# Performance work log

Hardware: AMD Instinct MI355X
Metric: run time of the kernel (lower is better)

Reference implementation:

```python
import jax, jax.numpy as jnp
import numpy as np

B, T, I, H = 512, 512, 64, 256


def _gru_layer(x, w_ih, w_hh, b_ih, b_hh):
    # x: [B, T, in]; w_ih: [3H, in]; w_hh: [3H, H]; gate order r, z, n (PyTorch)
    xg = jnp.einsum('bti,gi->btg', x, w_ih) + b_ih  # [B, T, 3H], input projections for all steps
    xg = jnp.swapaxes(xg, 0, 1)  # [T, B, 3H] for scan over time
    h0 = jnp.zeros((x.shape[0], w_hh.shape[1]), dtype=x.dtype)

    def step(h, xg_t):
        hg = h @ w_hh.T + b_hh  # [B, 3H]
        xr, xz, xn = jnp.split(xg_t, 3, axis=-1)
        hr, hz, hn = jnp.split(hg, 3, axis=-1)
        r = jax.nn.sigmoid(xr + hr)
        z = jax.nn.sigmoid(xz + hz)
        n = jnp.tanh(xn + r * hn)
        h_new = (1.0 - z) * n + z * h
        return h_new, h_new

    h_last, ys = jax.lax.scan(step, h0, xg)
    return jnp.swapaxes(ys, 0, 1), h_last  # [B, T, H], [B, H]


def setup_inputs() -> dict:
    key = jax.random.key(0)
    ks = jax.random.split(key, 11)
    s_in = 1.0 / np.sqrt(H)
    x = jax.random.normal(ks[0], (B, T, I), dtype=jnp.float32)
    w_ih0 = jax.random.uniform(ks[1], (3 * H, I), jnp.float32, -s_in, s_in)
    w_hh0 = jax.random.uniform(ks[2], (3 * H, H), jnp.float32, -s_in, s_in)
    b_ih0 = jax.random.uniform(ks[3], (3 * H,), jnp.float32, -s_in, s_in)
    b_hh0 = jax.random.uniform(ks[4], (3 * H,), jnp.float32, -s_in, s_in)
    w_ih1 = jax.random.uniform(ks[5], (3 * H, H), jnp.float32, -s_in, s_in)
    w_hh1 = jax.random.uniform(ks[6], (3 * H, H), jnp.float32, -s_in, s_in)
    b_ih1 = jax.random.uniform(ks[7], (3 * H,), jnp.float32, -s_in, s_in)
    b_hh1 = jax.random.uniform(ks[8], (3 * H,), jnp.float32, -s_in, s_in)
    w_lin = jax.random.uniform(ks[9], (1, H), jnp.float32, -s_in, s_in)
    b_lin = jax.random.uniform(ks[10], (1,), jnp.float32, -s_in, s_in)
    return dict(x=x, w_ih0=w_ih0, w_hh0=w_hh0, b_ih0=b_ih0, b_hh0=b_hh0,
                w_ih1=w_ih1, w_hh1=w_hh1, b_ih1=b_ih1, b_hh1=b_hh1,
                w_lin=w_lin, b_lin=b_lin)


def reference(x, w_ih0, w_hh0, b_ih0, b_hh0, w_ih1, w_hh1, b_ih1, b_hh1, w_lin, b_lin):
    y0, h_last0 = _gru_layer(x, w_ih0, w_hh0, b_ih0, b_hh0)
    # dropout(0.2) between layers is inactive at inference -> identity
    y1, h_last1 = _gru_layer(y0, w_ih1, w_hh1, b_ih1, b_hh1)
    # original uses hn[0] = final hidden of LAYER 0
    logits = (h_last0 @ w_lin.T + b_lin).reshape(-1)  # [B]
    p = jax.nn.sigmoid(logits)
    out = jnp.stack((p, 1.0 - p), axis=1).reshape(-1)  # [2B]
    return out
```

## Files before the change

### kernel.cpp

```cpp
#include <hip/hip_runtime.h>


typedef __attribute__((ext_vector_type(8))) short short8;
typedef __attribute__((ext_vector_type(4))) float floatx4;

#define T_LEN 512
#define I_DIM 64
#define H_DIM 256
#define NB 16
#define NWG 32
#define L2E 1.4426950408889634f

#define HSTATE_OFF 131072
#define XG_OFF     1048576
#define XG_PER_T   786432ull
#define XG_TSTRIDE 393216

__device__ __forceinline__ unsigned short f2bf(float f) {
    union { float f; unsigned u; } v; v.f = f;
    return (unsigned short)((v.u + 0x7FFFu + ((v.u >> 16) & 1u)) >> 16);
}

__device__ __forceinline__ float bf2f(unsigned short u) {
    union { unsigned u; float f; } v; v.u = ((unsigned)u) << 16;
    return v.f;
}

__device__ __forceinline__ short8 pack8v(floatx4 a, floatx4 b) {
    short8 r;
    r[0] = (short)f2bf(a[0]); r[1] = (short)f2bf(a[1]);
    r[2] = (short)f2bf(a[2]); r[3] = (short)f2bf(a[3]);
    r[4] = (short)f2bf(b[0]); r[5] = (short)f2bf(b[1]);
    r[6] = (short)f2bf(b[2]); r[7] = (short)f2bf(b[3]);
    return r;
}

__device__ __forceinline__ short8 pack8s(const float* p, float s) {
    floatx4 a = *(const floatx4*)p;
    floatx4 b = *(const floatx4*)(p + 4);
    short8 r;
    r[0] = (short)f2bf(a[0] * s); r[1] = (short)f2bf(a[1] * s);
    r[2] = (short)f2bf(a[2] * s); r[3] = (short)f2bf(a[3] * s);
    r[4] = (short)f2bf(b[0] * s); r[5] = (short)f2bf(b[1] * s);
    r[6] = (short)f2bf(b[2] * s); r[7] = (short)f2bf(b[3] * s);
    return r;
}

__device__ __forceinline__ float sigm(float a) {
    return 1.0f / (1.0f + __expf(-a));
}

__global__ void cvt_wih_kernel(const float* __restrict__ w,
                               unsigned short* __restrict__ o) {
    int i = blockIdx.x * 256 + threadIdx.x;
    if (i < 6144) {
        const int l  = i & 63;
        const int kx = (i >> 6) & 1;
        const int g  = (i >> 7) % 6;
        const int wv = (i >> 7) / 6;
        const int row = (g >> 1) * 256 + wv * 32 + (g & 1) * 16 + (l & 15);
        const int col = kx * 32 + (l >> 4) * 8;
        const float* p = w + row * I_DIM + col;
        *(short8*)&o[i * 8] = pack8v(*(const floatx4*)p,
                                     *(const floatx4*)(p + 4));
    }
}

__global__ __launch_bounds__(256) void xg_kernel(
    const float* __restrict__ x,
    const unsigned short* __restrict__ wih_bf,
    unsigned short* __restrict__ xg,
    const float* __restrict__ b_ih,
    const float* __restrict__ b_hh,
    int t0)
{
    const int tid  = threadIdx.x;
    const int wv   = tid >> 6;
    const int lane = tid & 63;
    const int m16  = lane & 15;
    const int quad = lane >> 4;
    const int wgb  = blockIdx.x & 31;
    const int tl0  = (blockIdx.x >> 5) * 16 + wv * 4;

    short8 af0[4], af1[4];
    #pragma unroll
    for (int j = 0; j < 4; ++j) {
        const float* xp = x + ((long)(wgb * 16 + m16) * T_LEN + (t0 + tl0 + j))
                              * I_DIM + quad * 8;
        af0[j] = pack8v(*(const floatx4*)xp,        *(const floatx4*)(xp + 4));
        af1[j] = pack8v(*(const floatx4*)(xp + 32), *(const floatx4*)(xp + 36));
    }

    #pragma unroll 1
    for (int wp = 0; wp < 8; ++wp) {
        #pragma unroll 1
        for (int gate = 0; gate < 3; ++gate) {
            const int u0 = wp * 32 + m16;
            float bs0, bs1, sc;
            if (gate < 2) {
                bs0 = b_ih[gate * 256 + u0]      + b_hh[gate * 256 + u0];
                bs1 = b_ih[gate * 256 + u0 + 16] + b_hh[gate * 256 + u0 + 16];
                sc  = L2E;
            } else {
                bs0 = b_ih[512 + u0];
                bs1 = b_ih[512 + u0 + 16];
                sc  = 2.0f * L2E;
            }
            const int gb = (wp * 6 + gate * 2) * 2;
            short8 b00 = *(const short8*)&wih_bf[((gb + 0) * 64 + lane) * 8];
            short8 b01 = *(const short8*)&wih_bf[((gb + 1) * 64 + lane) * 8];
            short8 b10 = *(const short8*)&wih_bf[((gb + 2) * 64 + lane) * 8];
            short8 b11 = *(const short8*)&wih_bf[((gb + 3) * 64 + lane) * 8];
            #pragma unroll
            for (int j = 0; j < 4; ++j) {
                floatx4 a0 = {0, 0, 0, 0}, a1 = {0, 0, 0, 0};
                a0 = __builtin_amdgcn_mfma_f32_16x16x32_bf16(af0[j], b00, a0, 0, 0, 0);
                a0 = __builtin_amdgcn_mfma_f32_16x16x32_bf16(af1[j], b01, a0, 0, 0, 0);
                a1 = __builtin_amdgcn_mfma_f32_16x16x32_bf16(af0[j], b10, a1, 0, 0, 0);
                a1 = __builtin_amdgcn_mfma_f32_16x16x32_bf16(af1[j], b11, a1, 0, 0, 0);
                short8 pk;
                pk[0] = (short)f2bf((a0[0] + bs0) * sc);
                pk[1] = (short)f2bf((a0[1] + bs0) * sc);
                pk[2] = (short)f2bf((a0[2] + bs0) * sc);
                pk[3] = (short)f2bf((a0[3] + bs0) * sc);
                pk[4] = (short)f2bf((a1[0] + bs1) * sc);
                pk[5] = (short)f2bf((a1[1] + bs1) * sc);
                pk[6] = (short)f2bf((a1[2] + bs1) * sc);
                pk[7] = (short)f2bf((a1[3] + bs1) * sc);
                long off = ((((long)(tl0 + j) * 32 + wgb) * 3 + gate) * 512
                            + wp * 64 + lane) * 8;
                *(short8*)&xg[off] = pk;
            }
        }
    }
}

__global__ __launch_bounds__(512, 2) void gru_scan8(
    const unsigned short* __restrict__ xg,
    const float* __restrict__ w_hh,
    const float* __restrict__ b_hh,
    const float* __restrict__ w_lin,
    const float* __restrict__ b_lin,
    float* __restrict__ h_state,
    float* __restrict__ out,
    int t0, int tlen, int last)
{
    __shared__ __align__(16) unsigned short hbf[1024 * 8];

    const int tid  = threadIdx.x;
    const int wave = tid >> 6;
    const int lane = tid & 63;
    const int m16  = lane & 15;
    const int quad = lane >> 4;
    const int wg   = blockIdx.x;

    for (int b = tid; b < 1024; b += 512)
        *(short8*)&hbf[b * 8] = (short8)0;

    float h_old[8] = {0, 0, 0, 0, 0, 0, 0, 0};
    if (t0 > 0) {
        unsigned short* hbn = &hbf[(t0 & 1) * 512 * 8];
        #pragma unroll
        for (int i = 0; i < 2; ++i) {
            #pragma unroll
            for (int r = 0; r < 4; ++r) {
                float v = h_state[(long)(wg * NB + quad * 4 + r) * H_DIM
                                  + wave * 32 + i * 16 + m16];
                h_old[i * 4 + r] = v;
                hbn[(wave * 64 + (i * 2 + (m16 >> 3)) * 16 + quad * 4 + r) * 8
                    + (m16 & 7)] = f2bf(v);
            }
        }
    }

    short8 whh[3][2][8];
    #pragma unroll
    for (int g = 0; g < 3; ++g) {
        const float sc = (g < 2) ? L2E : 2.0f * L2E;
        #pragma unroll
        for (int i = 0; i < 2; ++i) {
            const float* rp = w_hh
                + (long)(g * 256 + wave * 32 + i * 16 + m16) * H_DIM;
            #pragma unroll
            for (int k = 0; k < 8; ++k)
                whh[g][i][k] = pack8s(rp + k * 32 + quad * 8, sc);
        }
    }
    float anb[2];
    anb[0] = 2.0f * L2E * b_hh[512 + wave * 32 + m16];
    anb[1] = 2.0f * L2E * b_hh[512 + wave * 32 + 16 + m16];

    const unsigned short* xgb = xg + (long)wg * 12288 + tid * 8;
    short8 pf0 = *(const short8*)&xgb[0];
    short8 pf1 = *(const short8*)&xgb[4096];
    short8 xnc = *(const short8*)&xgb[8192];
    const unsigned short* xgn = xgb + XG_TSTRIDE;

    if (wave >= 4) __builtin_amdgcn_s_setprio(1);

    __syncthreads();

    #pragma unroll 1
    for (int tt = 0; tt < tlen; ++tt) {
        const int t = t0 + tt;
        floatx4 aR[2], aZ[2], aN[2];
        #pragma unroll
        for (int i = 0; i < 2; ++i) {
            #pragma unroll
            for (int r = 0; r < 4; ++r) {
                aR[i][r] = bf2f((unsigned short)pf0[i * 4 + r]);
                aZ[i][r] = bf2f((unsigned short)pf1[i * 4 + r]);
            }
            aN[i] = (floatx4){anb[i], anb[i], anb[i], anb[i]};
        }
        pf0 = *(const short8*)&xgn[0];
        pf1 = *(const short8*)&xgn[4096];

        const unsigned short* hb = &hbf[(t & 1) * 512 * 8];

        #pragma unroll
        for (int k = 0; k < 8; ++k) {
            short8 af = *(const short8*)&hb[(k * 64 + lane) * 8];
            aR[0] = __builtin_amdgcn_mfma_f32_16x16x32_bf16(af, whh[0][0][k], aR[0], 0, 0, 0);
            aR[1] = __builtin_amdgcn_mfma_f32_16x16x32_bf16(af, whh[0][1][k], aR[1], 0, 0, 0);
            aZ[0] = __builtin_amdgcn_mfma_f32_16x16x32_bf16(af, whh[1][0][k], aZ[0], 0, 0, 0);
            aZ[1] = __builtin_amdgcn_mfma_f32_16x16x32_bf16(af, whh[1][1][k], aZ[1], 0, 0, 0);
        }

        #pragma unroll
        for (int k = 0; k < 8; ++k) {
            short8 af = *(const short8*)&hb[(k * 64 + lane) * 8];
            aN[0] = __builtin_amdgcn_mfma_f32_16x16x32_bf16(af, whh[2][0][k], aN[0], 0, 0, 0);
            aN[1] = __builtin_amdgcn_mfma_f32_16x16x32_bf16(af, whh[2][1][k], aN[1], 0, 0, 0);
        }

        float rr[8], zh[8], omz[8], xf[8];
        #pragma unroll
        for (int i = 0; i < 2; ++i) {
            #pragma unroll
            for (int r = 0; r < 4; ++r) {
                const int e = i * 4 + r;
                rr[e]  = __builtin_amdgcn_rcpf(1.0f + __builtin_amdgcn_exp2f(-aR[i][r]));
                float zz = __builtin_amdgcn_rcpf(1.0f + __builtin_amdgcn_exp2f(-aZ[i][r]));
                zh[e]  = zz * h_old[e];
                omz[e] = 1.0f - zz;
                xf[e]  = bf2f((unsigned short)xnc[i * 4 + r]);
            }
        }

        unsigned short* hbn = &hbf[((t + 1) & 1) * 512 * 8];
        #pragma unroll
        for (int i = 0; i < 2; ++i) {
            float hv0, hv1, hv2, hv3;
            #pragma unroll
            for (int r = 0; r < 4; ++r) {
                const int e = i * 4 + r;
                float av = xf[e] + rr[e] * aN[i][r];
                float tn = 1.0f - 2.0f * __builtin_amdgcn_rcpf(1.0f + __builtin_amdgcn_exp2f(av));
                float hv = omz[e] * tn + zh[e];
                h_old[e] = hv;
                if (r == 0) hv0 = hv; else if (r == 1) hv1 = hv;
                else if (r == 2) hv2 = hv; else hv3 = hv;
            }
            unsigned pk0, pk1;
            asm("v_cvt_pk_bf16_f32 %0, %1, %2" : "=v"(pk0) : "v"(hv0), "v"(hv1));
            asm("v_cvt_pk_bf16_f32 %0, %1, %2" : "=v"(pk1) : "v"(hv2), "v"(hv3));
            unsigned short* wb = &hbn[(wave * 64 + (i * 2 + (m16 >> 3)) * 16
                                       + quad * 4) * 8 + (m16 & 7)];
            wb[0]  = (unsigned short)(pk0 & 0xffffu);
            wb[8]  = (unsigned short)(pk0 >> 16);
            wb[16] = (unsigned short)(pk1 & 0xffffu);
            wb[24] = (unsigned short)(pk1 >> 16);
        }

        xnc = *(const short8*)&xgn[8192];
        if (tt < tlen - 2) xgn += XG_TSTRIDE;

        asm volatile("s_waitcnt lgkmcnt(0)" ::: "memory");
        __builtin_amdgcn_s_barrier();
    }

    if (wave >= 4) __builtin_amdgcn_s_setprio(0);

    #pragma unroll
    for (int i = 0; i < 2; ++i)
        #pragma unroll
        for (int r = 0; r < 4; ++r)
            h_state[(long)(wg * NB + quad * 4 + r) * H_DIM
                    + wave * 32 + i * 16 + m16] = h_old[i * 4 + r];

    if (!last) return;

    __syncthreads();
    float* hfin = (float*)hbf;
    #pragma unroll
    for (int i = 0; i < 2; ++i)
        #pragma unroll
        for (int r = 0; r < 4; ++r)
            hfin[(quad * 4 + r) * 256 + wave * 32 + i * 16 + m16] =
                h_old[i * 4 + r];
    __syncthreads();

    const int m = tid >> 5, j = tid & 31;
    float s = 0.0f;
    #pragma unroll
    for (int c = 0; c < 8; ++c)
        s += hfin[m * 256 + j + c * 32] * w_lin[j + c * 32];
    #pragma unroll
    for (int d = 16; d > 0; d >>= 1) s += __shfl_down(s, d, 32);
    if (j == 0) {
        float p = sigm(s + b_lin[0]);
        const int b = wg * NB + m;
        out[2 * b]     = p;
        out[2 * b + 1] = 1.0f - p;
    }
}

__global__ __launch_bounds__(512, 1) void gru_kernel(
    const float* __restrict__ x,
    const float* __restrict__ w_hh,
    const float* __restrict__ b_ih,
    const float* __restrict__ b_hh,
    const unsigned short* __restrict__ wih_ws,
    const float* __restrict__ w_lin,
    const float* __restrict__ b_lin,
    float* __restrict__ out)
{
    __shared__ __align__(16) unsigned short whn_lds[8192 * 8];
    __shared__ __align__(16) unsigned short hbf[1024 * 8];
    __shared__ __align__(16) unsigned short bias_lds[512 * 8];

    const int tid  = threadIdx.x;
    const int wave = tid >> 6;
    const int lane = tid & 63;
    const int m16  = lane & 15;
    const int quad = lane >> 4;
    const int wg   = blockIdx.x;

    for (int b = tid; b < 8192; b += 512) {
        const int l = b & 63;
        const int k = (b >> 6) & 7;
        const int g = (b >> 9) & 1;
        const int w = b >> 10;
        const int row = 512 + w * 32 + g * 16 + (l & 15);
        const int col = k * 32 + (l >> 4) * 8;
        const float* p = w_hh + row * H_DIM + col;
        *(short8*)&whn_lds[b * 8] = pack8v(*(const floatx4*)p,
                                           *(const floatx4*)(p + 4));
    }
    for (int b = tid; b < 1024; b += 512)
        *(short8*)&hbf[b * 8] = (short8)0;

    {
        const int u0 = wave * 32 + m16, u1 = u0 + 16;
        unsigned short* bl = &bias_lds[tid * 8];
        bl[0] = f2bf(b_ih[u0] + b_hh[u0]);
        bl[1] = f2bf(b_ih[u1] + b_hh[u1]);
        bl[2] = f2bf(b_ih[256 + u0] + b_hh[256 + u0]);
        bl[3] = f2bf(b_ih[256 + u1] + b_hh[256 + u1]);
        bl[4] = f2bf(b_hh[512 + u0]);
        bl[5] = f2bf(b_hh[512 + u1]);
        bl[6] = f2bf(b_ih[512 + u0]);
        bl[7] = f2bf(b_ih[512 + u1]);
    }

    short8 whh[4][8];
    #pragma unroll
    for (int g = 0; g < 4; ++g) {
        const int row = (g >> 1) * 256 + wave * 32 + (g & 1) * 16 + m16;
        const float* rp = w_hh + row * H_DIM;
        #pragma unroll
        for (int k = 0; k < 8; ++k) {
            const float* p = rp + k * 32 + quad * 8;
            whh[g][k] = pack8v(*(const floatx4*)p, *(const floatx4*)(p + 4));
        }
    }

    short8 wi[12];
    {
        const unsigned short* wib = &wih_ws[(wave * 6 * 2 * 64 + lane) * 8];
        #pragma unroll
        for (int j = 0; j < 12; ++j)
            wi[j] = *(const short8*)&wib[j * 64 * 8];
    }

    float h_old[8] = {0, 0, 0, 0, 0, 0, 0, 0};
    const float* xbase = x + (long)(wg * NB + m16) * T_LEN * I_DIM + quad * 8;

    __syncthreads();

    #pragma unroll 1
    for (int t = 0; t < T_LEN; ++t) {
        const float* xt = xbase + t * I_DIM;
        floatx4 x0 = *(const floatx4*)(xt);
        floatx4 x1 = *(const floatx4*)(xt + 4);
        floatx4 x2 = *(const floatx4*)(xt + 32);
        floatx4 x3 = *(const floatx4*)(xt + 36);

        floatx4 acc[4], an[2], xnl[2];
        #pragma unroll
        for (int g = 0; g < 4; ++g) acc[g] = (floatx4){0, 0, 0, 0};
        an[0] = an[1] = xnl[0] = xnl[1] = (floatx4){0, 0, 0, 0};

        const unsigned short* hb  = &hbf[(t & 1) * 512 * 8];
        const unsigned short* wnb = &whn_lds[(wave * 2 * 8 * 64 + lane) * 8];
        #pragma unroll
        for (int k = 0; k < 8; ++k) {
            short8 af  = *(const short8*)&hb[(k * 64 + lane) * 8];
            short8 wn0 = *(const short8*)&wnb[(k * 64) * 8];
            short8 wn1 = *(const short8*)&wnb[((8 + k) * 64) * 8];
            acc[0] = __builtin_amdgcn_mfma_f32_16x16x32_bf16(af, whh[0][k], acc[0], 0, 0, 0);
            acc[1] = __builtin_amdgcn_mfma_f32_16x16x32_bf16(af, whh[1][k], acc[1], 0, 0, 0);
            acc[2] = __builtin_amdgcn_mfma_f32_16x16x32_bf16(af, whh[2][k], acc[2], 0, 0, 0);
            acc[3] = __builtin_amdgcn_mfma_f32_16x16x32_bf16(af, whh[3][k], acc[3], 0, 0, 0);
            an[0]  = __builtin_amdgcn_mfma_f32_16x16x32_bf16(af, wn0, an[0], 0, 0, 0);
            an[1]  = __builtin_amdgcn_mfma_f32_16x16x32_bf16(af, wn1, an[1], 0, 0, 0);
        }

        short8 xa = pack8v(x0, x1);
        acc[0] = __builtin_amdgcn_mfma_f32_16x16x32_bf16(xa, wi[0],  acc[0], 0, 0, 0);
        acc[1] = __builtin_amdgcn_mfma_f32_16x16x32_bf16(xa, wi[2],  acc[1], 0, 0, 0);
        acc[2] = __builtin_amdgcn_mfma_f32_16x16x32_bf16(xa, wi[4],  acc[2], 0, 0, 0);
        acc[3] = __builtin_amdgcn_mfma_f32_16x16x32_bf16(xa, wi[6],  acc[3], 0, 0, 0);
        xnl[0] = __builtin_amdgcn_mfma_f32_16x16x32_bf16(xa, wi[8],  xnl[0], 0, 0, 0);
        xnl[1] = __builtin_amdgcn_mfma_f32_16x16x32_bf16(xa, wi[10], xnl[1], 0, 0, 0);
        xa = pack8v(x2, x3);
        acc[0] = __builtin_amdgcn_mfma_f32_16x16x32_bf16(xa, wi[1],  acc[0], 0, 0, 0);
        acc[1] = __builtin_amdgcn_mfma_f32_16x16x32_bf16(xa, wi[3],  acc[1], 0, 0, 0);
        acc[2] = __builtin_amdgcn_mfma_f32_16x16x32_bf16(xa, wi[5],  acc[2], 0, 0, 0);
        acc[3] = __builtin_amdgcn_mfma_f32_16x16x32_bf16(xa, wi[7],  acc[3], 0, 0, 0);
        xnl[0] = __builtin_amdgcn_mfma_f32_16x16x32_bf16(xa, wi[9],  xnl[0], 0, 0, 0);
        xnl[1] = __builtin_amdgcn_mfma_f32_16x16x32_bf16(xa, wi[11], xnl[1], 0, 0, 0);

        short8 bv = *(const short8*)&bias_lds[tid * 8];
        unsigned short* hbn = &hbf[((t + 1) & 1) * 512 * 8];
        #pragma unroll
        for (int i = 0; i < 2; ++i) {
            #pragma unroll
            for (int r = 0; r < 4; ++r) {
                const int idx = i * 4 + r;
                float rr = sigm(acc[i][r]     + bf2f((unsigned short)bv[i]));
                float zz = sigm(acc[2 + i][r] + bf2f((unsigned short)bv[2 + i]));
                float av = xnl[i][r] + bf2f((unsigned short)bv[6 + i])
                         + rr * (an[i][r] + bf2f((unsigned short)bv[4 + i]));
                float nn = 1.0f - 2.0f / (1.0f + __expf(2.0f * av));
                float hn = (1.0f - zz) * nn + zz * h_old[idx];
                h_old[idx] = hn;
                hbn[(wave * 64 + (i * 2 + (m16 >> 3)) * 16 + quad * 4 + r) * 8
                    + (m16 & 7)] = f2bf(hn);
            }
        }
        __syncthreads();
    }

    __syncthreads();
    float* hfin = (float*)hbf;
    #pragma unroll
    for (int i = 0; i < 2; ++i)
        #pragma unroll
        for (int r = 0; r < 4; ++r)
            hfin[(quad * 4 + r) * 256 + wave * 32 + i * 16 + m16] =
                h_old[i * 4 + r];
    __syncthreads();

    const int m = tid >> 5, j = tid & 31;
    float s = 0.0f;
    #pragma unroll
    for (int c = 0; c < 8; ++c)
        s += hfin[m * 256 + j + c * 32] * w_lin[j + c * 32];
    #pragma unroll
    for (int d = 16; d > 0; d >>= 1) s += __shfl_down(s, d, 32);
    if (j == 0) {
        float p = sigm(s + b_lin[0]);
        const int b = wg * NB + m;
        out[2 * b]     = p;
        out[2 * b + 1] = 1.0f - p;
    }
}

extern "C" void kernel_launch(void* const* d_in, const int* in_sizes, int n_in,
                              void* d_out, int out_size, void* d_ws, size_t ws_size,
                              hipStream_t stream) {
    const float* x     = (const float*)d_in[0];
    const float* w_ih0 = (const float*)d_in[1];
    const float* w_hh0 = (const float*)d_in[2];
    const float* b_ih0 = (const float*)d_in[3];
    const float* b_hh0 = (const float*)d_in[4];
    const float* w_lin = (const float*)d_in[9];
    const float* b_lin = (const float*)d_in[10];
    float* out = (float*)d_out;

    unsigned short* wih_bf = (unsigned short*)d_ws;
    cvt_wih_kernel<<<24, 256, 0, stream>>>(w_ih0, wih_bf);

    int Tc = 0;
    for (int c = 512; c >= 32; c >>= 1)
        if (ws_size >= XG_OFF + (size_t)c * XG_PER_T) { Tc = c; break; }

    if (Tc) {
        float* h_state = (float*)((char*)d_ws + HSTATE_OFF);
        unsigned short* xg = (unsigned short*)((char*)d_ws + XG_OFF);
        for (int t0 = 0; t0 < T_LEN; t0 += Tc) {
            xg_kernel<<<32 * (Tc / 16), 256, 0, stream>>>(x, wih_bf, xg,
                                                          b_ih0, b_hh0, t0);
            gru_scan8<<<NWG, 512, 0, stream>>>(xg, w_hh0, b_hh0,
                                               w_lin, b_lin, h_state, out,
                                               t0, Tc, (t0 + Tc == T_LEN) ? 1 : 0);
        }
    } else {
        gru_kernel<<<NWG, 512, 0, stream>>>(x, w_hh0, b_ih0, b_hh0, wih_bf,
                                            w_lin, b_lin, out);
    }
}
```

Before: 1.037 ms.

## Overlap next-chunk input projection with GRU scan using extra producer workgroups

The scan kernel is launched with 256 workgroups. The first 32 run the recurrent scan over the current time chunk, and the rest compute the bf16 input projections for the next chunk into a second, double-buffered xg region. This hides the separate xg_kernel launches behind the latency-bound scan, which uses only 32 CUs. The sigmoid for r/z is also moved before the n-gate MFMAs, the h update is simplified to tn + z*(h - tn), and wave priority setting is dropped. It needs twice the xg workspace and caps chunks at 256, which means more scan launches, and producer waves may compete with scan workgroups for bandwidth.

```diff
diff --git a/kernel.cpp b/kernel.cpp
--- a/kernel.cpp
+++ b/kernel.cpp
@@ -66,21 +66,16 @@
     }
 }
 
-__global__ __launch_bounds__(256) void xg_kernel(
+__device__ __forceinline__ void xg_produce_wave(
     const float* __restrict__ x,
     const unsigned short* __restrict__ wih_bf,
     unsigned short* __restrict__ xg,
     const float* __restrict__ b_ih,
     const float* __restrict__ b_hh,
-    int t0)
+    int t0, int tl0, int wgb, int lane)
 {
-    const int tid  = threadIdx.x;
-    const int wv   = tid >> 6;
-    const int lane = tid & 63;
     const int m16  = lane & 15;
     const int quad = lane >> 4;
-    const int wgb  = blockIdx.x & 31;
-    const int tl0  = (blockIdx.x >> 5) * 16 + wv * 4;
 
     short8 af0[4], af1[4];
     #pragma unroll
@@ -135,10 +130,30 @@
     }
 }
 
+__global__ __launch_bounds__(256) void xg_kernel(
+    const float* __restrict__ x,
+    const unsigned short* __restrict__ wih_bf,
+    unsigned short* __restrict__ xg,
+    const float* __restrict__ b_ih,
+    const float* __restrict__ b_hh,
+    int t0)
+{
+    const int tid  = threadIdx.x;
+    const int wv   = tid >> 6;
+    const int lane = tid & 63;
+    const int wgb  = blockIdx.x & 31;
+    const int tl0  = (blockIdx.x >> 5) * 16 + wv * 4;
+    xg_produce_wave(x, wih_bf, xg, b_ih, b_hh, t0, tl0, wgb, lane);
+}
+
 __global__ __launch_bounds__(512, 2) void gru_scan8(
     const unsigned short* __restrict__ xg,
+    unsigned short* __restrict__ xg_next,
+    const float* __restrict__ x,
+    const unsigned short* __restrict__ wih_bf,
+    const float* __restrict__ b_ih,
+    const float* __restrict__ b_hh,
     const float* __restrict__ w_hh,
-    const float* __restrict__ b_hh,
     const float* __restrict__ w_lin,
     const float* __restrict__ b_lin,
     float* __restrict__ h_state,
@@ -154,6 +169,18 @@
     const int quad = lane >> 4;
     const int wg   = blockIdx.x;
 
+    if (wg >= NWG) {
+        const int t0n = t0 + tlen;
+        if (xg_next != nullptr && t0n < T_LEN) {
+            const int nwaves = (gridDim.x - NWG) * 8;
+            const int ntask  = 32 * (tlen >> 2);
+            for (int task = (wg - NWG) * 8 + wave; task < ntask; task += nwaves)
+                xg_produce_wave(x, wih_bf, xg_next, b_ih, b_hh,
+                                t0n, (task >> 5) * 4, task & 31, lane);
+        }
+        return;
+    }
+
     for (int b = tid; b < 1024; b += 512)
         *(short8*)&hbf[b * 8] = (short8)0;
 
@@ -196,8 +223,6 @@
     short8 xnc = *(const short8*)&xgb[8192];
     const unsigned short* xgn = xgb + XG_TSTRIDE;
 
-    if (wave >= 4) __builtin_amdgcn_s_setprio(1);
-
     __syncthreads();
 
     #pragma unroll 1
@@ -228,36 +253,32 @@
         }
 
         #pragma unroll
+        for (int i = 0; i < 2; ++i) {
+            #pragma unroll
+            for (int r = 0; r < 4; ++r) {
+                aR[i][r] = __builtin_amdgcn_rcpf(1.0f + __builtin_amdgcn_exp2f(-aR[i][r]));
+                aZ[i][r] = __builtin_amdgcn_rcpf(1.0f + __builtin_amdgcn_exp2f(-aZ[i][r]));
+            }
+        }
+
+        #pragma unroll
         for (int k = 0; k < 8; ++k) {
             short8 af = *(const short8*)&hb[(k * 64 + lane) * 8];
             aN[0] = __builtin_amdgcn_mfma_f32_16x16x32_bf16(af, whh[2][0][k], aN[0], 0, 0, 0);
             aN[1] = __builtin_amdgcn_mfma_f32_16x16x32_bf16(af, whh[2][1][k], aN[1], 0, 0, 0);
         }
 
-        float rr[8], zh[8], omz[8], xf[8];
+        unsigned short* hbn = &hbf[((t + 1) & 1) * 512 * 8];
         #pragma unroll
         for (int i = 0; i < 2; ++i) {
+            float hv0, hv1, hv2, hv3;
             #pragma unroll
             for (int r = 0; r < 4; ++r) {
                 const int e = i * 4 + r;
-                rr[e]  = __builtin_amdgcn_rcpf(1.0f + __builtin_amdgcn_exp2f(-aR[i][r]));
-                float zz = __builtin_amdgcn_rcpf(1.0f + __builtin_amdgcn_exp2f(-aZ[i][r]));
-                zh[e]  = zz * h_old[e];
-                omz[e] = 1.0f - zz;
-                xf[e]  = bf2f((unsigned short)xnc[i * 4 + r]);
-            }
-        }
-
-        unsigned short* hbn = &hbf[((t + 1) & 1) * 512 * 8];
-        #pragma unroll
-        for (int i = 0; i < 2; ++i) {
-            float hv0, hv1, hv2, hv3;
-            #pragma unroll
-            for (int r = 0; r < 4; ++r) {
-                const int e = i * 4 + r;
-                float av = xf[e] + rr[e] * aN[i][r];
+                float xnv = bf2f((unsigned short)xnc[i * 4 + r]);
+                float av = xnv + aR[i][r] * aN[i][r];
                 float tn = 1.0f - 2.0f * __builtin_amdgcn_rcpf(1.0f + __builtin_amdgcn_exp2f(av));
-                float hv = omz[e] * tn + zh[e];
+                float hv = tn + aZ[i][r] * (h_old[e] - tn);
                 h_old[e] = hv;
                 if (r == 0) hv0 = hv; else if (r == 1) hv1 = hv;
                 else if (r == 2) hv2 = hv; else hv3 = hv;
@@ -279,8 +300,6 @@
         asm volatile("s_waitcnt lgkmcnt(0)" ::: "memory");
         __builtin_amdgcn_s_barrier();
     }
-
-    if (wave >= 4) __builtin_amdgcn_s_setprio(0);
 
     #pragma unroll
     for (int i = 0; i < 2; ++i)
@@ -493,19 +512,45 @@
     unsigned short* wih_bf = (unsigned short*)d_ws;
     cvt_wih_kernel<<<24, 256, 0, stream>>>(w_ih0, wih_bf);
 
+    float* h_state = (float*)((char*)d_ws + HSTATE_OFF);
+
+    int Tc2 = 0;
+    for (int c = 256; c >= 32; c >>= 1)
+        if (ws_size >= XG_OFF + 2ull * c * XG_PER_T) { Tc2 = c; break; }
+
+    if (Tc2) {
+        unsigned short* xgA = (unsigned short*)((char*)d_ws + XG_OFF);
+        unsigned short* xgB = xgA + (size_t)Tc2 * (XG_PER_T / 2);
+        xg_kernel<<<32 * (Tc2 / 16), 256, 0, stream>>>(x, wih_bf, xgA,
+                                                       b_ih0, b_hh0, 0);
+        int par = 0;
+        for (int t0 = 0; t0 < T_LEN; t0 += Tc2) {
+            unsigned short* cur = par ? xgB : xgA;
+            unsigned short* nxt = par ? xgA : xgB;
+            gru_scan8<<<256, 512, 0, stream>>>(cur, nxt, x, wih_bf,
+                                               b_ih0, b_hh0, w_hh0,
+                                               w_lin, b_lin, h_state, out,
+                                               t0, Tc2,
+                                               (t0 + Tc2 >= T_LEN) ? 1 : 0);
+            par ^= 1;
+        }
+        return;
+    }
+
     int Tc = 0;
-    for (int c = 512; c >= 32; c >>= 1)
+    for (int c = 256; c >= 32; c >>= 1)
         if (ws_size >= XG_OFF + (size_t)c * XG_PER_T) { Tc = c; break; }
 
     if (Tc) {
-        float* h_state = (float*)((char*)d_ws + HSTATE_OFF);
         unsigned short* xg = (unsigned short*)((char*)d_ws + XG_OFF);
         for (int t0 = 0; t0 < T_LEN; t0 += Tc) {
             xg_kernel<<<32 * (Tc / 16), 256, 0, stream>>>(x, wih_bf, xg,
                                                           b_ih0, b_hh0, t0);
-            gru_scan8<<<NWG, 512, 0, stream>>>(xg, w_hh0, b_hh0,
+            gru_scan8<<<NWG, 512, 0, stream>>>(xg, nullptr, x, wih_bf,
+                                               b_ih0, b_hh0, w_hh0,
                                                w_lin, b_lin, h_state, out,
-                                               t0, Tc, (t0 + Tc == T_LEN) ? 1 : 0);
+                                               t0, Tc,
+                                               (t0 + Tc >= T_LEN) ? 1 : 0);
         }
     } else {
         gru_kernel<<<NWG, 512, 0, stream>>>(x, w_hh0, b_ih0, b_hh0, wih_bf,
```

New measurement: 1.008 ms. -2.8%, faster.
